# Kernel optimization log

Measured on AMD Instinct MI355X. Metric: run time of the kernel, lower is better.

## Reference

```python
import jax, jax.numpy as jnp
import numpy as np

B, C, H, W = 8, 512, 64, 64
K = 8  # shrink factor: qk channels = C//K, v channels = C//2


def conv1x1(x, w, b):
    # x: [B,C_in,H,W], w: [C_out,C_in], b: [C_out]  (1x1 conv == channel matmul)
    return jnp.einsum('bchw,oc->bohw', x, w) + b[None, :, None, None]


def maxpool2x2(x):
    b, c, h, w = x.shape
    return x.reshape(b, c, h // 2, 2, w // 2, 2).max(axis=(3, 5))


def setup_inputs() -> dict:
    key = jax.random.key(0)
    ks = jax.random.split(key, 9)
    Cqk, Cv = C // K, C // 2
    sc = lambda fan_in: 1.0 / np.sqrt(fan_in)
    return {
        'x': jax.random.normal(ks[0], (B, C, H, W), jnp.float32),
        'Wf': jax.random.normal(ks[1], (Cqk, C), jnp.float32) * sc(C),
        'bf': jnp.zeros((Cqk,), jnp.float32),
        'Wg': jax.random.normal(ks[2], (Cqk, C), jnp.float32) * sc(C),
        'bg': jnp.zeros((Cqk,), jnp.float32),
        'Wh': jax.random.normal(ks[3], (Cv, C), jnp.float32) * sc(C),
        'bh': jnp.zeros((Cv,), jnp.float32),
        'Wv': jax.random.normal(ks[4], (C, Cv), jnp.float32) * sc(Cv),
        'bv': jnp.zeros((C,), jnp.float32),
        'gamma': jnp.float32(0.5),
    }


def reference(x, Wf, bf, Wg, bg, Wh, bh, Wv, bv, gamma):
    b, c, h, w = x.shape
    f = conv1x1(x, Wf, bf).reshape(b, c // K, h * w)          # [B, C/K, HW]
    g = maxpool2x2(conv1x1(x, Wg, bg))                         # [B, C/K, H/2, W/2]
    v = maxpool2x2(conv1x1(x, Wh, bh))                         # [B, C/2, H/2, W/2]
    hwp = (h // 2) * (w // 2)
    g = g.reshape(b, c // K, hwp)
    v = v.reshape(b, c // 2, hwp)
    # s[b, n, m] = sum_c f[b,c,n] g[b,c,m]; softmax over m (no scaling, per SAGAN)
    s = jnp.einsum('bcn,bcm->bnm', f, g)                       # [B, HW, HW']
    beta = jax.nn.softmax(s, axis=-1)
    o = jnp.einsum('bcm,bnm->bcn', v, beta).reshape(b, c // 2, h, w)
    return gamma * conv1x1(o, Wv, bv) + x
```

## Files before the change

### kernel.cpp

```cpp
#include <hip/hip_runtime.h>
#include <cstddef>

typedef __attribute__((ext_vector_type(4))) float f32x4;
typedef __attribute__((ext_vector_type(16))) float f32x16;
typedef __attribute__((ext_vector_type(8))) short bf16x8;

#define MFMA16(A, B, C) __builtin_amdgcn_mfma_f32_16x16x32_bf16(A, B, C, 0, 0, 0)
#define MFMA32(A, B, C) __builtin_amdgcn_mfma_f32_32x32x16_bf16(A, B, C, 0, 0, 0)

__device__ __forceinline__ unsigned short f2bf(float f) {
  unsigned u = __float_as_uint(f);
  u += 0x7fffu + ((u >> 16) & 1u);
  return (unsigned short)(u >> 16);
}
__device__ __forceinline__ float bf2f(unsigned short s) {
  return __uint_as_float(((unsigned)s) << 16);
}

__device__ __forceinline__ void cvt_split8(float4 a, float4 b, bf16x8* H, bf16x8* L) {
  float v[8] = {a.x, a.y, a.z, a.w, b.x, b.y, b.z, b.w};
  unsigned hh[4], ll[4];
  #pragma unroll
  for (int p = 0; p < 4; ++p) {
    unsigned short h0 = f2bf(v[2 * p]), h1 = f2bf(v[2 * p + 1]);
    hh[p] = (unsigned)h0 | ((unsigned)h1 << 16);
    unsigned short l0 = f2bf(v[2 * p] - bf2f(h0));
    unsigned short l1 = f2bf(v[2 * p + 1] - bf2f(h1));
    ll[p] = (unsigned)l0 | ((unsigned)l1 << 16);
  }
  uint4 uh; uh.x = hh[0]; uh.y = hh[1]; uh.z = hh[2]; uh.w = hh[3];
  uint4 ul; ul.x = ll[0]; ul.y = ll[1]; ul.z = ll[2]; ul.w = ll[3];
  *H = *(bf16x8*)&uh;
  *L = *(bf16x8*)&ul;
}

__device__ __forceinline__ bf16x8 cvt_hi8(float4 a, float4 b) {
  float v[8] = {a.x, a.y, a.z, a.w, b.x, b.y, b.z, b.w};
  unsigned hh[4];
  #pragma unroll
  for (int p = 0; p < 4; ++p)
    hh[p] = (unsigned)f2bf(v[2 * p]) | ((unsigned)f2bf(v[2 * p + 1]) << 16);
  uint4 uh; uh.x = hh[0]; uh.y = hh[1]; uh.z = hh[2]; uh.w = hh[3];
  return *(bf16x8*)&uh;
}


__global__ void prep_k(const float* __restrict__ Wf, const float* __restrict__ Wg,
                       const float* __restrict__ Wh, const float* __restrict__ Wv,
                       unsigned short* __restrict__ wfh, unsigned short* __restrict__ wfl,
                       unsigned short* __restrict__ wgh, unsigned short* __restrict__ wgl,
                       unsigned short* __restrict__ whb, unsigned short* __restrict__ wvb) {
  int i = blockIdx.x * 256 + threadIdx.x;
  if (i < 65536) {
    int ii = i & 32767;
    int j = ii & 7, slot = (ii >> 3) & 63, q = slot & 15, qt2 = slot >> 4;
    int kt = (ii >> 9) & 15, oct = ii >> 13;
    const float* src = (i < 32768) ? Wf : Wg;
    unsigned short* dh = (i < 32768) ? wfh : wgh;
    unsigned short* dl = (i < 32768) ? wfl : wgl;
    float v = src[(oct * 16 + q) * 512 + kt * 32 + qt2 * 8 + j];
    unsigned short h = f2bf(v);
    dh[ii] = h; dl[ii] = f2bf(v - bf2f(h));
  } else if (i < 196608) {
    int ii = i - 65536;
    int j = ii & 7, slot = (ii >> 3) & 63, q = slot & 15, qt2 = slot >> 4;
    int kt = (ii >> 9) & 15, oct = ii >> 13;
    whb[ii] = f2bf(Wh[(oct * 16 + q) * 512 + kt * 32 + qt2 * 8 + j]);
  } else if (i < 327680) {
    int ii = i - 196608;
    int j = ii & 7, slot = (ii >> 3) & 63, q = slot & 15, qt2 = slot >> 4;
    int kt = (ii >> 9) & 7, oct = ii >> 12;
    wvb[ii] = f2bf(Wv[(oct * 16 + q) * 256 + kt * 32 + qt2 * 8 + j]);
  }
}


#define STAGE(BUF, CN) { _Pragma("unroll") \
  for (int c_ = 0; c_ < 8; ++c_) { \
    __builtin_amdgcn_global_load_lds( \
      (const __attribute__((address_space(1))) unsigned int*)(xg + (size_t)((CN) * 64 + c_ * 2) * 4096), \
      (__attribute__((address_space(3))) unsigned int*)(&xs[BUF][w * 16 + c_ * 2][0]), \
      16, 0, 0); } }

__global__ __launch_bounds__(256, 2)
void conv_all(const float* __restrict__ x,
              const unsigned short* __restrict__ wfh_, const unsigned short* __restrict__ wfl_,
              const unsigned short* __restrict__ wgh_, const unsigned short* __restrict__ wgl_,
              const unsigned short* __restrict__ whb_,
              const float* __restrict__ bf_, const float* __restrict__ bg_,
              const float* __restrict__ bh_,
              unsigned short* __restrict__ fhi, unsigned short* __restrict__ flo,
              unsigned short* __restrict__ ghi, unsigned short* __restrict__ glo,
              unsigned short* __restrict__ vp)
{
  __shared__ __align__(16) float xs[2][64][128];
  const int bid = blockIdx.x;
  const int b = bid & 7;
  const int idx = bid >> 3;
  const int role = idx & 1;
  const int hp = idx >> 1;
  const int n0 = hp * 128;
  const int tid = threadIdx.x, w = tid >> 6, lane = tid & 63, q = lane & 15, qt = lane >> 4;
  const float* xg = x + ((size_t)(b * 512 + w * 16 + (lane >> 5)) * 4096) + n0 + (lane & 31) * 4;

  if (role == 0) {
    f32x4 accf[2][4], accg[2][4];
    #pragma unroll
    for (int nt = 0; nt < 2; ++nt)
      #pragma unroll
      for (int ot = 0; ot < 4; ++ot) {
        accf[nt][ot] = (f32x4){0.f, 0.f, 0.f, 0.f};
        accg[nt][ot] = (f32x4){0.f, 0.f, 0.f, 0.f};
      }
    STAGE(0, 0)
    __syncthreads();
    for (int cc = 0; cc < 8; ++cc) {
      const int cur = cc & 1;
      if (cc < 7) STAGE(cur ^ 1, cc + 1)
      #pragma unroll
      for (int kh = 0; kh < 2; ++kh) {
        const int kt = cc * 2 + kh;
        bf16x8 Ah[2], Al[2];
        #pragma unroll
        for (int nt = 0; nt < 2; ++nt) {
          const int row = w * 32 + nt * 16 + q;
          float xv[8];
          #pragma unroll
          for (int j = 0; j < 8; ++j)
            xv[j] = xs[cur][kh * 32 + qt * 8 + j][row];
          float4 a0; a0.x = xv[0]; a0.y = xv[1]; a0.z = xv[2]; a0.w = xv[3];
          float4 a1; a1.x = xv[4]; a1.y = xv[5]; a1.z = xv[6]; a1.w = xv[7];
          cvt_split8(a0, a1, &Ah[nt], &Al[nt]);
        }
        {
          bf16x8 Bh[4], Bl[4];
          #pragma unroll
          for (int ot = 0; ot < 4; ++ot) {
            size_t wb = ((size_t)(ot * 16 + kt) << 9) + lane * 8;
            Bh[ot] = *(const bf16x8*)(wfh_ + wb);
            Bl[ot] = *(const bf16x8*)(wfl_ + wb);
          }
          #pragma unroll
          for (int nt = 0; nt < 2; ++nt)
            #pragma unroll
            for (int ot = 0; ot < 4; ++ot) {
              accf[nt][ot] = MFMA16(Ah[nt], Bh[ot], accf[nt][ot]);
              accf[nt][ot] = MFMA16(Ah[nt], Bl[ot], accf[nt][ot]);
              accf[nt][ot] = MFMA16(Al[nt], Bh[ot], accf[nt][ot]);
            }
        }
        {
          bf16x8 Bh[4], Bl[4];
          #pragma unroll
          for (int ot = 0; ot < 4; ++ot) {
            size_t wb = ((size_t)(ot * 16 + kt) << 9) + lane * 8;
            Bh[ot] = *(const bf16x8*)(wgh_ + wb);
            Bl[ot] = *(const bf16x8*)(wgl_ + wb);
          }
          #pragma unroll
          for (int nt = 0; nt < 2; ++nt)
            #pragma unroll
            for (int ot = 0; ot < 4; ++ot) {
              accg[nt][ot] = MFMA16(Ah[nt], Bh[ot], accg[nt][ot]);
              accg[nt][ot] = MFMA16(Ah[nt], Bl[ot], accg[nt][ot]);
              accg[nt][ot] = MFMA16(Al[nt], Bh[ot], accg[nt][ot]);
            }
        }
      }
      __syncthreads();
    }
    #pragma unroll
    for (int nt = 0; nt < 2; ++nt)
      #pragma unroll
      for (int ot = 0; ot < 4; ++ot)
        #pragma unroll
        for (int r = 0; r < 4; ++r) {
          float v = accf[nt][ot][r] + bf_[ot * 16 + q];
          unsigned short h = f2bf(v);
          size_t o = (((size_t)(b * 128 + hp * 4 + w) * 4 + ot) * 64 +
                      (q >> 3) * 32 + nt * 16 + qt * 4 + r) * 8 + (q & 7);
          fhi[o] = h;
          flo[o] = f2bf(v - bf2f(h));
        }
    float (*pl)[67] = (float(*)[67])&xs[0][0][0];
    #pragma unroll
    for (int nt = 0; nt < 2; ++nt)
      #pragma unroll
      for (int ot = 0; ot < 4; ++ot)
        #pragma unroll
        for (int r = 0; r < 4; ++r)
          pl[w * 32 + nt * 16 + qt * 4 + r][ot * 16 + q] = accg[nt][ot][r];
    __syncthreads();
    const int c = tid & 63;
    #pragma unroll
    for (int it = 0; it < 8; ++it) {
      int wp = (tid >> 6) + it * 4;
      float v = fmaxf(fmaxf(pl[2 * wp][c], pl[2 * wp + 1][c]),
                      fmaxf(pl[64 + 2 * wp][c], pl[65 + 2 * wp][c])) + bg_[c];
      unsigned short h = f2bf(v);
      size_t o = (((size_t)(b * 32 + hp) * 4 + (c >> 4)) * 64 +
                  ((c >> 3) & 1) * 32 + wp) * 8 + (c & 7);
      ghi[o] = h;
      glo[o] = f2bf(v - bf2f(h));
    }
  } else {
    f32x4 acc[2][16];
    #pragma unroll
    for (int nt = 0; nt < 2; ++nt)
      #pragma unroll
      for (int ot = 0; ot < 16; ++ot) acc[nt][ot] = (f32x4){0.f, 0.f, 0.f, 0.f};
    STAGE(0, 0)
    __syncthreads();
    for (int cc = 0; cc < 8; ++cc) {
      const int cur = cc & 1;
      if (cc < 7) STAGE(cur ^ 1, cc + 1)
      #pragma unroll
      for (int kh = 0; kh < 2; ++kh) {
        const int kt = cc * 2 + kh;
        bf16x8 A_[2];
        #pragma unroll
        for (int nt = 0; nt < 2; ++nt) {
          const int row = w * 32 + nt * 16 + q;
          float xv[8];
          #pragma unroll
          for (int j = 0; j < 8; ++j)
            xv[j] = xs[cur][kh * 32 + qt * 8 + j][row];
          float4 a0; a0.x = xv[0]; a0.y = xv[1]; a0.z = xv[2]; a0.w = xv[3];
          float4 a1; a1.x = xv[4]; a1.y = xv[5]; a1.z = xv[6]; a1.w = xv[7];
          A_[nt] = cvt_hi8(a0, a1);
        }
        #pragma unroll
        for (int oh = 0; oh < 2; ++oh) {
          bf16x8 B_[8];
          #pragma unroll
          for (int ot = 0; ot < 8; ++ot)
            B_[ot] = *(const bf16x8*)(whb_ + ((size_t)((oh * 8 + ot) * 16 + kt) << 9) + lane * 8);
          #pragma unroll
          for (int nt = 0; nt < 2; ++nt)
            #pragma unroll
            for (int ot = 0; ot < 8; ++ot)
              acc[nt][oh * 8 + ot] = MFMA16(A_[nt], B_[ot], acc[nt][oh * 8 + ot]);
        }
      }
      __syncthreads();
    }
    float (*pl)[67] = (float(*)[67])&xs[0][0][0];
    #pragma unroll
    for (int oh = 0; oh < 4; ++oh) {
      if (oh) __syncthreads();
      #pragma unroll
      for (int nt = 0; nt < 2; ++nt)
        #pragma unroll
        for (int ot4 = 0; ot4 < 4; ++ot4)
          #pragma unroll
          for (int r = 0; r < 4; ++r)
            pl[w * 32 + nt * 16 + qt * 4 + r][ot4 * 16 + q] = acc[nt][oh * 4 + ot4][r];
      __syncthreads();
      const int wp = tid & 31;
      #pragma unroll
      for (int it = 0; it < 8; ++it) {
        int cc2 = (tid >> 5) + it * 8;
        int cv = oh * 64 + cc2;
        float v = fmaxf(fmaxf(pl[2 * wp][cc2], pl[2 * wp + 1][cc2]),
                        fmaxf(pl[64 + 2 * wp][cc2], pl[65 + 2 * wp][cc2])) + bh_[cv];
        size_t o = (((size_t)(b * 16 + (cv >> 4)) * 32 + hp) * 64 +
                    (wp >> 3) * 16 + (cv & 15)) * 8 + (wp & 7);
        vp[o] = f2bf(v);
      }
    }
  }
}


#define PROW 264

__global__ __launch_bounds__(256, 2)
void attn_mfma(const unsigned short* __restrict__ f_, const unsigned short* __restrict__ fl_,
               const unsigned short* __restrict__ g_, const unsigned short* __restrict__ gl_,
               const unsigned short* __restrict__ vp, unsigned short* __restrict__ oT)
{
  __shared__ __align__(16) unsigned short PB[64 * PROW];
  __shared__ float redm[4][2][32], reds[4][2][32];
  const int b = blockIdx.x & 7, bx = blockIdx.x >> 3;
  const int tid = threadIdx.x, w = tid >> 6, lane = tid & 63;
  const int q32 = lane & 31, hl = lane >> 5;
  const int q16 = lane & 15, qt = lane >> 4;

  bf16x8 Fh[2][4], Fl[2][4];
  #pragma unroll
  for (int qt2 = 0; qt2 < 2; ++qt2) {
    size_t fb = ((size_t)(b * 128 + bx * 2 + qt2) << 11) + lane * 8;
    #pragma unroll
    for (int s = 0; s < 4; ++s) {
      Fh[qt2][s] = *(const bf16x8*)(f_ + fb + (s << 9));
      Fl[qt2][s] = *(const bf16x8*)(fl_ + fb + (s << 9));
    }
  }

  float M0 = -3.0e38f, M1 = -3.0e38f;
  float Mp[4], Sp[4];
  #pragma unroll
  for (int qs = 0; qs < 4; ++qs) { Mp[qs] = -3.0e38f; Sp[qs] = 0.f; }
  f32x4 oacc[4][4];
  #pragma unroll
  for (int c4 = 0; c4 < 4; ++c4)
    #pragma unroll
    for (int qs = 0; qs < 4; ++qs) oacc[c4][qs] = (f32x4){0.f, 0.f, 0.f, 0.f};
  const size_t vroot = ((size_t)(b * 16 + w * 4) * 32) * 512 + lane * 8;

#define VLD(C4, KS) (*(const bf16x8*)(vp + vroot + ((size_t)((C4) * 32 + mc * 8 + (KS)) << 9)))
#define LOADVA(KS) { va0 = VLD(0, KS); va1 = VLD(1, KS); va2 = VLD(2, KS); va3 = VLD(3, KS); }
#define LOADVB(KS) { vb0 = VLD(0, KS); vb1 = VLD(1, KS); vb2 = VLD(2, KS); vb3 = VLD(3, KS); }
#define PVMFMA(KS, V0, V1, V2, V3) { \
  bf16x8 pb0 = *(const bf16x8*)&PB[q16 * PROW + (KS) * 32 + qt * 8]; \
  bf16x8 pb1 = *(const bf16x8*)&PB[(16 + q16) * PROW + (KS) * 32 + qt * 8]; \
  bf16x8 pb2 = *(const bf16x8*)&PB[(32 + q16) * PROW + (KS) * 32 + qt * 8]; \
  bf16x8 pb3 = *(const bf16x8*)&PB[(48 + q16) * PROW + (KS) * 32 + qt * 8]; \
  oacc[0][0] = MFMA16(V0, pb0, oacc[0][0]); oacc[1][0] = MFMA16(V1, pb0, oacc[1][0]); \
  oacc[2][0] = MFMA16(V2, pb0, oacc[2][0]); oacc[3][0] = MFMA16(V3, pb0, oacc[3][0]); \
  oacc[0][1] = MFMA16(V0, pb1, oacc[0][1]); oacc[1][1] = MFMA16(V1, pb1, oacc[1][1]); \
  oacc[2][1] = MFMA16(V2, pb1, oacc[2][1]); oacc[3][1] = MFMA16(V3, pb1, oacc[3][1]); \
  oacc[0][2] = MFMA16(V0, pb2, oacc[0][2]); oacc[1][2] = MFMA16(V1, pb2, oacc[1][2]); \
  oacc[2][2] = MFMA16(V2, pb2, oacc[2][2]); oacc[3][2] = MFMA16(V3, pb2, oacc[3][2]); \
  oacc[0][3] = MFMA16(V0, pb3, oacc[0][3]); oacc[1][3] = MFMA16(V1, pb3, oacc[1][3]); \
  oacc[2][3] = MFMA16(V2, pb3, oacc[2][3]); oacc[3][3] = MFMA16(V3, pb3, oacc[3][3]); }

  #pragma unroll 1
  for (int mc = 0; mc < 4; ++mc) {
    f32x16 sa0t0 = {}, sa0t1 = {}, sa1t0 = {}, sa1t1 = {};
    __builtin_amdgcn_s_setprio(1);
    #pragma unroll
    for (int t = 0; t < 2; ++t) {
      size_t gb = ((size_t)(b * 32 + mc * 8 + w * 2 + t) << 11) + lane * 8;
      bf16x8 Gh[4], Gl[4];
      #pragma unroll
      for (int s = 0; s < 4; ++s) {
        Gh[s] = *(const bf16x8*)(g_ + gb + (s << 9));
        Gl[s] = *(const bf16x8*)(gl_ + gb + (s << 9));
      }
      f32x16* s0 = t ? &sa0t1 : &sa0t0;
      f32x16* s1 = t ? &sa1t1 : &sa1t0;
      #pragma unroll
      for (int s = 0; s < 4; ++s) {
        *s0 = MFMA32(Gh[s], Fh[0][s], *s0);
        *s0 = MFMA32(Gh[s], Fl[0][s], *s0);
        *s0 = MFMA32(Gl[s], Fh[0][s], *s0);
        *s1 = MFMA32(Gh[s], Fh[1][s], *s1);
        *s1 = MFMA32(Gh[s], Fl[1][s], *s1);
        *s1 = MFMA32(Gl[s], Fh[1][s], *s1);
      }
    }
    __builtin_amdgcn_s_setprio(0);

    bf16x8 va0, va1, va2, va3, vb0, vb1, vb2, vb3;
    LOADVA(0)

    float mx0 = -3.0e38f, mx1 = -3.0e38f;
    #pragma unroll
    for (int r = 0; r < 16; ++r) {
      mx0 = fmaxf(mx0, fmaxf(sa0t0[r], sa0t1[r]));
      mx1 = fmaxf(mx1, fmaxf(sa1t0[r], sa1t1[r]));
    }
    mx0 = fmaxf(mx0, __shfl_xor(mx0, 32));
    mx1 = fmaxf(mx1, __shfl_xor(mx1, 32));
    if (lane < 32) { redm[w][0][lane] = mx0; redm[w][1][lane] = mx1; }
    __syncthreads();
    float gmx0 = fmaxf(fmaxf(redm[0][0][q32], redm[1][0][q32]), fmaxf(redm[2][0][q32], redm[3][0][q32]));
    float gmx1 = fmaxf(fmaxf(redm[0][1][q32], redm[1][1][q32]), fmaxf(redm[2][1][q32], redm[3][1][q32]));
    float Mn0 = fmaxf(M0, gmx0), Mn1 = fmaxf(M1, gmx1);
    M0 = Mn0; M1 = Mn1;

    float rfp[4];
    #pragma unroll
    for (int qs = 0; qs < 4; ++qs) {
      int hq = qs >> 1, cq = (qs & 1) * 16 + q16;
      float gm = fmaxf(fmaxf(redm[0][hq][cq], redm[1][hq][cq]),
                       fmaxf(redm[2][hq][cq], redm[3][hq][cq]));
      float Mn = fmaxf(Mp[qs], gm);
      rfp[qs] = __expf(Mp[qs] - Mn);
      Mp[qs] = Mn;
    }

    float cs0 = 0.f, cs1 = 0.f;
    #pragma unroll
    for (int r = 0; r < 16; ++r) {
      float p;
      p = __expf(sa0t0[r] - Mn0); sa0t0[r] = p; cs0 += p;
      p = __expf(sa0t1[r] - Mn0); sa0t1[r] = p; cs0 += p;
      p = __expf(sa1t0[r] - Mn1); sa1t0[r] = p; cs1 += p;
      p = __expf(sa1t1[r] - Mn1); sa1t1[r] = p; cs1 += p;
    }
    cs0 += __shfl_xor(cs0, 32);
    cs1 += __shfl_xor(cs1, 32);
    if (lane < 32) { reds[w][0][lane] = cs0; reds[w][1][lane] = cs1; }

    #pragma unroll
    for (int j = 0; j < 4; ++j) {
      uint2 pk;
      pk.x = (unsigned)f2bf(sa0t0[4*j+0]) | ((unsigned)f2bf(sa0t0[4*j+1]) << 16);
      pk.y = (unsigned)f2bf(sa0t0[4*j+2]) | ((unsigned)f2bf(sa0t0[4*j+3]) << 16);
      *(uint2*)&PB[q32 * PROW + w * 64 + j * 8 + hl * 4] = pk;
      pk.x = (unsigned)f2bf(sa0t1[4*j+0]) | ((unsigned)f2bf(sa0t1[4*j+1]) << 16);
      pk.y = (unsigned)f2bf(sa0t1[4*j+2]) | ((unsigned)f2bf(sa0t1[4*j+3]) << 16);
      *(uint2*)&PB[q32 * PROW + w * 64 + 32 + j * 8 + hl * 4] = pk;
      pk.x = (unsigned)f2bf(sa1t0[4*j+0]) | ((unsigned)f2bf(sa1t0[4*j+1]) << 16);
      pk.y = (unsigned)f2bf(sa1t0[4*j+2]) | ((unsigned)f2bf(sa1t0[4*j+3]) << 16);
      *(uint2*)&PB[(32 + q32) * PROW + w * 64 + j * 8 + hl * 4] = pk;
      pk.x = (unsigned)f2bf(sa1t1[4*j+0]) | ((unsigned)f2bf(sa1t1[4*j+1]) << 16);
      pk.y = (unsigned)f2bf(sa1t1[4*j+2]) | ((unsigned)f2bf(sa1t1[4*j+3]) << 16);
      *(uint2*)&PB[(32 + q32) * PROW + w * 64 + 32 + j * 8 + hl * 4] = pk;
    }
    __syncthreads();

    #pragma unroll
    for (int qs = 0; qs < 4; ++qs) {
      int hq = qs >> 1, cq = (qs & 1) * 16 + q16;
      float ct = reds[0][hq][cq] + reds[1][hq][cq] + reds[2][hq][cq] + reds[3][hq][cq];
      Sp[qs] = (mc == 0) ? ct : Sp[qs] * rfp[qs] + ct;
    }

    if (mc > 0) {
      #pragma unroll
      for (int c4 = 0; c4 < 4; ++c4)
        #pragma unroll
        for (int qs = 0; qs < 4; ++qs) oacc[c4][qs] *= rfp[qs];
    }
    LOADVB(1)
    __builtin_amdgcn_s_setprio(1);
    #pragma unroll
    for (int kp = 0; kp < 4; ++kp) {
      PVMFMA(2 * kp, va0, va1, va2, va3)
      if (2 * kp + 2 < 8) LOADVA(2 * kp + 2)
      PVMFMA(2 * kp + 1, vb0, vb1, vb2, vb3)
      if (2 * kp + 3 < 8) LOADVB(2 * kp + 3)
    }
    __builtin_amdgcn_s_setprio(0);
  }

  __syncthreads();
  float rinv[4];
  #pragma unroll
  for (int qs = 0; qs < 4; ++qs) rinv[qs] = 1.0f / Sp[qs];
  #pragma unroll
  for (int c4 = 0; c4 < 4; ++c4)
    #pragma unroll
    for (int qs = 0; qs < 4; ++qs) {
      uint2 pk;
      pk.x = (unsigned)f2bf(oacc[c4][qs][0] * rinv[qs]) | ((unsigned)f2bf(oacc[c4][qs][1] * rinv[qs]) << 16);
      pk.y = (unsigned)f2bf(oacc[c4][qs][2] * rinv[qs]) | ((unsigned)f2bf(oacc[c4][qs][3] * rinv[qs]) << 16);
      *(uint2*)&PB[(qs * 16 + q16) * PROW + w * 64 + c4 * 16 + qt * 4] = pk;
    }
  __syncthreads();
  const size_t obase = (size_t)(b * 256 + bx * 4) * 4096;
  #pragma unroll
  for (int it = 0; it < 8; ++it) {
    int u = it * 256 + tid;
    int so = u * 8;
    int ntl = so >> 12;
    int rem = so & 4095;
    int ks = rem >> 9;
    int slot = (rem >> 3) & 63;
    int qq = slot & 15, cg = slot >> 4;
    uint4 val = *(const uint4*)&PB[(ntl * 16 + qq) * PROW + ks * 32 + cg * 8];
    *(uint4*)(oT + obase + so) = val;
  }
}


__global__ __launch_bounds__(256)
void conv_final(const unsigned short* __restrict__ A, const unsigned short* __restrict__ W,
                const float* __restrict__ bias, float* __restrict__ out,
                const float* __restrict__ resid, const float* __restrict__ gamma_p)
{
  const int bid = blockIdx.x;
  const int b = bid & 7;
  const int idx = bid >> 3;
  const int n0 = (idx & 31) * 128;
  const int oc0 = (idx >> 5) * 128;
  const int tid = threadIdx.x, w = tid >> 6, lane = tid & 63, q = lane & 15, qt = lane >> 4;

  f32x4 acc[2][8];
  #pragma unroll
  for (int nt = 0; nt < 2; ++nt)
    #pragma unroll
    for (int ot = 0; ot < 8; ++ot) acc[nt][ot] = (f32x4){0.f, 0.f, 0.f, 0.f};

  #pragma unroll
  for (int ks = 0; ks < 8; ++ks) {
    bf16x8 A_[2], B_[8];
    #pragma unroll
    for (int nt = 0; nt < 2; ++nt)
      A_[nt] = *(const bf16x8*)(A + (((size_t)(b * 256 + (n0 >> 4) + w * 2 + nt) * 8 + ks) << 9) + lane * 8);
    #pragma unroll
    for (int ot = 0; ot < 8; ++ot)
      B_[ot] = *(const bf16x8*)(W + (((size_t)((oc0 >> 4) + ot) * 8 + ks) << 9) + lane * 8);
    #pragma unroll
    for (int nt = 0; nt < 2; ++nt)
      #pragma unroll
      for (int ot = 0; ot < 8; ++ot)
        acc[nt][ot] = MFMA16(A_[nt], B_[ot], acc[nt][ot]);
  }

  const float gm = gamma_p[0];
  #pragma unroll
  for (int ot = 0; ot < 8; ++ot) {
    int oc = oc0 + ot * 16 + q;
    float bs = bias[oc];
    #pragma unroll
    for (int nt = 0; nt < 2; ++nt) {
      int n = n0 + w * 32 + nt * 16 + qt * 4;
      size_t o = ((size_t)(b * 512) + oc) * 4096 + n;
      float4 rs = *(const float4*)&resid[o];
      float4 ov;
      ov.x = gm * (acc[nt][ot][0] + bs) + rs.x;
      ov.y = gm * (acc[nt][ot][1] + bs) + rs.y;
      ov.z = gm * (acc[nt][ot][2] + bs) + rs.z;
      ov.w = gm * (acc[nt][ot][3] + bs) + rs.w;
      *(float4*)&out[o] = ov;
    }
  }
}


extern "C" void kernel_launch(void* const* d_in, const int* in_sizes, int n_in,
                              void* d_out, int out_size, void* d_ws, size_t ws_size,
                              hipStream_t stream) {
  const float* x     = (const float*)d_in[0];
  const float* Wf    = (const float*)d_in[1];
  const float* bf    = (const float*)d_in[2];
  const float* Wg    = (const float*)d_in[3];
  const float* bg    = (const float*)d_in[4];
  const float* Wh    = (const float*)d_in[5];
  const float* bh    = (const float*)d_in[6];
  const float* Wv    = (const float*)d_in[7];
  const float* bv    = (const float*)d_in[8];
  const float* gamma = (const float*)d_in[9];
  float* out = (float*)d_out;
  char* w = (char*)d_ws;

  unsigned short* fhi = (unsigned short*)(w);
  unsigned short* flo = (unsigned short*)(w + 4194304);
  unsigned short* ghi = (unsigned short*)(w + 8388608);
  unsigned short* glo = (unsigned short*)(w + 9437184);
  unsigned short* vp  = (unsigned short*)(w + 10485760);
  unsigned short* oT  = (unsigned short*)(w + 14680064);
  unsigned short* wfh = (unsigned short*)(w + 31457280);
  unsigned short* wfl = (unsigned short*)(w + 31522816);
  unsigned short* wgh = (unsigned short*)(w + 31588352);
  unsigned short* wgl = (unsigned short*)(w + 31653888);
  unsigned short* whb = (unsigned short*)(w + 31719424);
  unsigned short* wvb = (unsigned short*)(w + 31981568);

  prep_k<<<1280, 256, 0, stream>>>(Wf, Wg, Wh, Wv, wfh, wfl, wgh, wgl, whb, wvb);

  conv_all<<<512, 256, 0, stream>>>(x, wfh, wfl, wgh, wgl, whb,
                                    bf, bg, bh, fhi, flo, ghi, glo, vp);

  attn_mfma<<<512, 256, 0, stream>>>(fhi, flo, ghi, glo, vp, oT);

  conv_final<<<1024, 256, 0, stream>>>(oT, wvb, bv, out, x, gamma);
}
```

Baseline: 111.3 us.

## Halve attention query tile to 32 rows and double grid for occupancy

The attention kernel now processes 32 query rows per block instead of 64, so it launches twice as many blocks, uses half the LDS and fewer accumulator registers, and raises the launch bound to 3 blocks per CU. The goal is better latency hiding and wave occupancy. In exchange, each block reloads the full G and V streams for half the queries, so global and L2 traffic for K/V doubles and each MFMA has less reuse.

Result: slower. 116.7 us (+4.8%).

```diff
diff --git a/kernel.cpp b/kernel.cpp
--- a/kernel.cpp
+++ b/kernel.cpp
@@ -274,38 +274,37 @@
 
 #define PROW 264
 
-__global__ __launch_bounds__(256, 2)
+__global__ __launch_bounds__(256, 3)
 void attn_mfma(const unsigned short* __restrict__ f_, const unsigned short* __restrict__ fl_,
                const unsigned short* __restrict__ g_, const unsigned short* __restrict__ gl_,
                const unsigned short* __restrict__ vp, unsigned short* __restrict__ oT)
 {
-  __shared__ __align__(16) unsigned short PB[64 * PROW];
-  __shared__ float redm[4][2][32], reds[4][2][32];
+  __shared__ __align__(16) unsigned short PB[32 * PROW];
+  __shared__ float redm[4][32], reds[4][32];
   const int b = blockIdx.x & 7, bx = blockIdx.x >> 3;
   const int tid = threadIdx.x, w = tid >> 6, lane = tid & 63;
   const int q32 = lane & 31, hl = lane >> 5;
   const int q16 = lane & 15, qt = lane >> 4;
 
-  bf16x8 Fh[2][4], Fl[2][4];
-  #pragma unroll
-  for (int qt2 = 0; qt2 < 2; ++qt2) {
-    size_t fb = ((size_t)(b * 128 + bx * 2 + qt2) << 11) + lane * 8;
+  bf16x8 Fh[4], Fl[4];
+  {
+    size_t fb = ((size_t)(b * 128 + bx) << 11) + lane * 8;
     #pragma unroll
     for (int s = 0; s < 4; ++s) {
-      Fh[qt2][s] = *(const bf16x8*)(f_ + fb + (s << 9));
-      Fl[qt2][s] = *(const bf16x8*)(fl_ + fb + (s << 9));
-    }
-  }
-
-  float M0 = -3.0e38f, M1 = -3.0e38f;
-  float Mp[4], Sp[4];
-  #pragma unroll
-  for (int qs = 0; qs < 4; ++qs) { Mp[qs] = -3.0e38f; Sp[qs] = 0.f; }
-  f32x4 oacc[4][4];
+      Fh[s] = *(const bf16x8*)(f_ + fb + (s << 9));
+      Fl[s] = *(const bf16x8*)(fl_ + fb + (s << 9));
+    }
+  }
+
+  float M0 = -3.0e38f;
+  float Mp[2], Sp[2];
+  #pragma unroll
+  for (int qs = 0; qs < 2; ++qs) { Mp[qs] = -3.0e38f; Sp[qs] = 0.f; }
+  f32x4 oacc[4][2];
   #pragma unroll
   for (int c4 = 0; c4 < 4; ++c4)
     #pragma unroll
-    for (int qs = 0; qs < 4; ++qs) oacc[c4][qs] = (f32x4){0.f, 0.f, 0.f, 0.f};
+    for (int qs = 0; qs < 2; ++qs) oacc[c4][qs] = (f32x4){0.f, 0.f, 0.f, 0.f};
   const size_t vroot = ((size_t)(b * 16 + w * 4) * 32) * 512 + lane * 8;
 
 #define VLD(C4, KS) (*(const bf16x8*)(vp + vroot + ((size_t)((C4) * 32 + mc * 8 + (KS)) << 9)))
@@ -314,20 +313,14 @@
 #define PVMFMA(KS, V0, V1, V2, V3) { \
   bf16x8 pb0 = *(const bf16x8*)&PB[q16 * PROW + (KS) * 32 + qt * 8]; \
   bf16x8 pb1 = *(const bf16x8*)&PB[(16 + q16) * PROW + (KS) * 32 + qt * 8]; \
-  bf16x8 pb2 = *(const bf16x8*)&PB[(32 + q16) * PROW + (KS) * 32 + qt * 8]; \
-  bf16x8 pb3 = *(const bf16x8*)&PB[(48 + q16) * PROW + (KS) * 32 + qt * 8]; \
   oacc[0][0] = MFMA16(V0, pb0, oacc[0][0]); oacc[1][0] = MFMA16(V1, pb0, oacc[1][0]); \
   oacc[2][0] = MFMA16(V2, pb0, oacc[2][0]); oacc[3][0] = MFMA16(V3, pb0, oacc[3][0]); \
   oacc[0][1] = MFMA16(V0, pb1, oacc[0][1]); oacc[1][1] = MFMA16(V1, pb1, oacc[1][1]); \
-  oacc[2][1] = MFMA16(V2, pb1, oacc[2][1]); oacc[3][1] = MFMA16(V3, pb1, oacc[3][1]); \
-  oacc[0][2] = MFMA16(V0, pb2, oacc[0][2]); oacc[1][2] = MFMA16(V1, pb2, oacc[1][2]); \
-  oacc[2][2] = MFMA16(V2, pb2, oacc[2][2]); oacc[3][2] = MFMA16(V3, pb2, oacc[3][2]); \
-  oacc[0][3] = MFMA16(V0, pb3, oacc[0][3]); oacc[1][3] = MFMA16(V1, pb3, oacc[1][3]); \
-  oacc[2][3] = MFMA16(V2, pb3, oacc[2][3]); oacc[3][3] = MFMA16(V3, pb3, oacc[3][3]); }
+  oacc[2][1] = MFMA16(V2, pb1, oacc[2][1]); oacc[3][1] = MFMA16(V3, pb1, oacc[3][1]); }
 
   #pragma unroll 1
   for (int mc = 0; mc < 4; ++mc) {
-    f32x16 sa0t0 = {}, sa0t1 = {}, sa1t0 = {}, sa1t1 = {};
+    f32x16 sat0 = {}, sat1 = {};
     __builtin_amdgcn_s_setprio(1);
     #pragma unroll
     for (int t = 0; t < 2; ++t) {
@@ -338,16 +331,12 @@
         Gh[s] = *(const bf16x8*)(g_ + gb + (s << 9));
         Gl[s] = *(const bf16x8*)(gl_ + gb + (s << 9));
       }
-      f32x16* s0 = t ? &sa0t1 : &sa0t0;
-      f32x16* s1 = t ? &sa1t1 : &sa1t0;
+      f32x16* s0 = t ? &sat1 : &sat0;
       #pragma unroll
       for (int s = 0; s < 4; ++s) {
-        *s0 = MFMA32(Gh[s], Fh[0][s], *s0);
-        *s0 = MFMA32(Gh[s], Fl[0][s], *s0);
-        *s0 = MFMA32(Gl[s], Fh[0][s], *s0);
-        *s1 = MFMA32(Gh[s], Fh[1][s], *s1);
-        *s1 = MFMA32(Gh[s], Fl[1][s], *s1);
-        *s1 = MFMA32(Gl[s], Fh[1][s], *s1);
+        *s0 = MFMA32(Gh[s], Fh[s], *s0);
+        *s0 = MFMA32(Gh[s], Fl[s], *s0);
+        *s0 = MFMA32(Gl[s], Fh[s], *s0);
       }
     }
     __builtin_amdgcn_s_setprio(0);
@@ -355,67 +344,54 @@
     bf16x8 va0, va1, va2, va3, vb0, vb1, vb2, vb3;
     LOADVA(0)
 
-    float mx0 = -3.0e38f, mx1 = -3.0e38f;
-    #pragma unroll
-    for (int r = 0; r < 16; ++r) {
-      mx0 = fmaxf(mx0, fmaxf(sa0t0[r], sa0t1[r]));
-      mx1 = fmaxf(mx1, fmaxf(sa1t0[r], sa1t1[r]));
-    }
+    float mx0 = -3.0e38f;
+    #pragma unroll
+    for (int r = 0; r < 16; ++r)
+      mx0 = fmaxf(mx0, fmaxf(sat0[r], sat1[r]));
     mx0 = fmaxf(mx0, __shfl_xor(mx0, 32));
-    mx1 = fmaxf(mx1, __shfl_xor(mx1, 32));
-    if (lane < 32) { redm[w][0][lane] = mx0; redm[w][1][lane] = mx1; }
+    if (lane < 32) redm[w][lane] = mx0;
     __syncthreads();
-    float gmx0 = fmaxf(fmaxf(redm[0][0][q32], redm[1][0][q32]), fmaxf(redm[2][0][q32], redm[3][0][q32]));
-    float gmx1 = fmaxf(fmaxf(redm[0][1][q32], redm[1][1][q32]), fmaxf(redm[2][1][q32], redm[3][1][q32]));
-    float Mn0 = fmaxf(M0, gmx0), Mn1 = fmaxf(M1, gmx1);
-    M0 = Mn0; M1 = Mn1;
-
-    float rfp[4];
-    #pragma unroll
-    for (int qs = 0; qs < 4; ++qs) {
-      int hq = qs >> 1, cq = (qs & 1) * 16 + q16;
-      float gm = fmaxf(fmaxf(redm[0][hq][cq], redm[1][hq][cq]),
-                       fmaxf(redm[2][hq][cq], redm[3][hq][cq]));
+    float gmx0 = fmaxf(fmaxf(redm[0][q32], redm[1][q32]), fmaxf(redm[2][q32], redm[3][q32]));
+    float Mn0 = fmaxf(M0, gmx0);
+    M0 = Mn0;
+
+    float rfp[2];
+    #pragma unroll
+    for (int qs = 0; qs < 2; ++qs) {
+      int cq = qs * 16 + q16;
+      float gm = fmaxf(fmaxf(redm[0][cq], redm[1][cq]),
+                       fmaxf(redm[2][cq], redm[3][cq]));
       float Mn = fmaxf(Mp[qs], gm);
       rfp[qs] = __expf(Mp[qs] - Mn);
       Mp[qs] = Mn;
     }
 
-    float cs0 = 0.f, cs1 = 0.f;
+    float cs0 = 0.f;
     #pragma unroll
     for (int r = 0; r < 16; ++r) {
       float p;
-      p = __expf(sa0t0[r] - Mn0); sa0t0[r] = p; cs0 += p;
-      p = __expf(sa0t1[r] - Mn0); sa0t1[r] = p; cs0 += p;
-      p = __expf(sa1t0[r] - Mn1); sa1t0[r] = p; cs1 += p;
-      p = __expf(sa1t1[r] - Mn1); sa1t1[r] = p; cs1 += p;
+      p = __expf(sat0[r] - Mn0); sat0[r] = p; cs0 += p;
+      p = __expf(sat1[r] - Mn0); sat1[r] = p; cs0 += p;
     }
     cs0 += __shfl_xor(cs0, 32);
-    cs1 += __shfl_xor(cs1, 32);
-    if (lane < 32) { reds[w][0][lane] = cs0; reds[w][1][lane] = cs1; }
+    if (lane < 32) reds[w][lane] = cs0;
 
     #pragma unroll
     for (int j = 0; j < 4; ++j) {
       uint2 pk;
-      pk.x = (unsigned)f2bf(sa0t0[4*j+0]) | ((unsigned)f2bf(sa0t0[4*j+1]) << 16);
-      pk.y = (unsigned)f2bf(sa0t0[4*j+2]) | ((unsigned)f2bf(sa0t0[4*j+3]) << 16);
+      pk.x = (unsigned)f2bf(sat0[4*j+0]) | ((unsigned)f2bf(sat0[4*j+1]) << 16);
+      pk.y = (unsigned)f2bf(sat0[4*j+2]) | ((unsigned)f2bf(sat0[4*j+3]) << 16);
       *(uint2*)&PB[q32 * PROW + w * 64 + j * 8 + hl * 4] = pk;
-      pk.x = (unsigned)f2bf(sa0t1[4*j+0]) | ((unsigned)f2bf(sa0t1[4*j+1]) << 16);
-      pk.y = (unsigned)f2bf(sa0t1[4*j+2]) | ((unsigned)f2bf(sa0t1[4*j+3]) << 16);
+      pk.x = (unsigned)f2bf(sat1[4*j+0]) | ((unsigned)f2bf(sat1[4*j+1]) << 16);
+      pk.y = (unsigned)f2bf(sat1[4*j+2]) | ((unsigned)f2bf(sat1[4*j+3]) << 16);
       *(uint2*)&PB[q32 * PROW + w * 64 + 32 + j * 8 + hl * 4] = pk;
-      pk.x = (unsigned)f2bf(sa1t0[4*j+0]) | ((unsigned)f2bf(sa1t0[4*j+1]) << 16);
-      pk.y = (unsigned)f2bf(sa1t0[4*j+2]) | ((unsigned)f2bf(sa1t0[4*j+3]) << 16);
-      *(uint2*)&PB[(32 + q32) * PROW + w * 64 + j * 8 + hl * 4] = pk;
-      pk.x = (unsigned)f2bf(sa1t1[4*j+0]) | ((unsigned)f2bf(sa1t1[4*j+1]) << 16);
-      pk.y = (unsigned)f2bf(sa1t1[4*j+2]) | ((unsigned)f2bf(sa1t1[4*j+3]) << 16);
-      *(uint2*)&PB[(32 + q32) * PROW + w * 64 + 32 + j * 8 + hl * 4] = pk;
     }
     __syncthreads();
 
     #pragma unroll
-    for (int qs = 0; qs < 4; ++qs) {
-      int hq = qs >> 1, cq = (qs & 1) * 16 + q16;
-      float ct = reds[0][hq][cq] + reds[1][hq][cq] + reds[2][hq][cq] + reds[3][hq][cq];
+    for (int qs = 0; qs < 2; ++qs) {
+      int cq = qs * 16 + q16;
+      float ct = reds[0][cq] + reds[1][cq] + reds[2][cq] + reds[3][cq];
       Sp[qs] = (mc == 0) ? ct : Sp[qs] * rfp[qs] + ct;
     }
 
@@ -423,7 +399,7 @@
       #pragma unroll
       for (int c4 = 0; c4 < 4; ++c4)
         #pragma unroll
-        for (int qs = 0; qs < 4; ++qs) oacc[c4][qs] *= rfp[qs];
+        for (int qs = 0; qs < 2; ++qs) oacc[c4][qs] *= rfp[qs];
     }
     LOADVB(1)
     __builtin_amdgcn_s_setprio(1);
@@ -438,22 +414,22 @@
   }
 
   __syncthreads();
-  float rinv[4];
-  #pragma unroll
-  for (int qs = 0; qs < 4; ++qs) rinv[qs] = 1.0f / Sp[qs];
+  float rinv[2];
+  #pragma unroll
+  for (int qs = 0; qs < 2; ++qs) rinv[qs] = 1.0f / Sp[qs];
   #pragma unroll
   for (int c4 = 0; c4 < 4; ++c4)
     #pragma unroll
-    for (int qs = 0; qs < 4; ++qs) {
+    for (int qs = 0; qs < 2; ++qs) {
       uint2 pk;
       pk.x = (unsigned)f2bf(oacc[c4][qs][0] * rinv[qs]) | ((unsigned)f2bf(oacc[c4][qs][1] * rinv[qs]) << 16);
       pk.y = (unsigned)f2bf(oacc[c4][qs][2] * rinv[qs]) | ((unsigned)f2bf(oacc[c4][qs][3] * rinv[qs]) << 16);
       *(uint2*)&PB[(qs * 16 + q16) * PROW + w * 64 + c4 * 16 + qt * 4] = pk;
     }
   __syncthreads();
-  const size_t obase = (size_t)(b * 256 + bx * 4) * 4096;
-  #pragma unroll
-  for (int it = 0; it < 8; ++it) {
+  const size_t obase = (size_t)(b * 256 + bx * 2) * 4096;
+  #pragma unroll
+  for (int it = 0; it < 4; ++it) {
     int u = it * 256 + tid;
     int so = u * 8;
     int ntl = so >> 12;
@@ -556,7 +532,7 @@
   conv_all<<<512, 256, 0, stream>>>(x, wfh, wfl, wgh, wgl, whb,
                                     bf, bg, bh, fhi, flo, ghi, glo, vp);
 
-  attn_mfma<<<512, 256, 0, stream>>>(fhi, flo, ghi, glo, vp, oT);
+  attn_mfma<<<1024, 256, 0, stream>>>(fhi, flo, ghi, glo, vp, oT);
 
   conv_final<<<1024, 256, 0, stream>>>(oT, wvb, bv, out, x, gamma);
 }
```

## Stage conv weight tiles into LDS via async global_load_lds alongside x

Applied to the files above, without the earlier changes.

The conv kernel used to read bf16 weight fragments directly from global memory inside the MFMA loop. It now copies each K-slice of weights into double-buffered LDS with global_load_lds, in step with the x tiles. The K chunk is halved to 32 channels per stage, giving 16 iterations instead of 8, so the same 64KB of LDS holds both x and weight buffers. This is meant to hide weight-load latency behind compute, at the cost of more barriers per K pass and a different LDS footprint.

Result: no change. 110.4 us (-0.8%).

```diff
diff --git a/kernel.cpp b/kernel.cpp
--- a/kernel.cpp
+++ b/kernel.cpp
@@ -7,6 +7,8 @@
 
 #define MFMA16(A, B, C) __builtin_amdgcn_mfma_f32_16x16x32_bf16(A, B, C, 0, 0, 0)
 #define MFMA32(A, B, C) __builtin_amdgcn_mfma_f32_32x32x16_bf16(A, B, C, 0, 0, 0)
+#define AS1 __attribute__((address_space(1)))
+#define AS3 __attribute__((address_space(3)))
 
 __device__ __forceinline__ unsigned short f2bf(float f) {
   unsigned u = __float_as_uint(f);
@@ -75,12 +77,25 @@
 }
 
 
-#define STAGE(BUF, CN) { _Pragma("unroll") \
-  for (int c_ = 0; c_ < 8; ++c_) { \
+#define STAGEX(XP, CN) { _Pragma("unroll") \
+  for (int c_ = 0; c_ < 4; ++c_) \
     __builtin_amdgcn_global_load_lds( \
-      (const __attribute__((address_space(1))) unsigned int*)(xg + (size_t)((CN) * 64 + c_ * 2) * 4096), \
-      (__attribute__((address_space(3))) unsigned int*)(&xs[BUF][w * 16 + c_ * 2][0]), \
-      16, 0, 0); } }
+      (const AS1 unsigned int*)(xg + (size_t)((CN) * 32 + c_ * 2) * 4096), \
+      (AS3 unsigned int*)((XP) + (w * 8 + c_ * 2) * 128), 16, 0, 0); }
+
+#define STAGEW0(WP, CN) { \
+  const unsigned short* Wt_ = (w == 0) ? wfh_ : (w == 1) ? wfl_ : (w == 2) ? wgh_ : wgl_; \
+  _Pragma("unroll") \
+  for (int ot_ = 0; ot_ < 4; ++ot_) \
+    __builtin_amdgcn_global_load_lds( \
+      (const AS1 unsigned int*)(Wt_ + (((size_t)(ot_ * 16 + (CN))) << 9) + lane * 8), \
+      (AS3 unsigned int*)((WP) + (w * 4 + ot_) * 512), 16, 0, 0); }
+
+#define STAGEW1(WP, CN) { _Pragma("unroll") \
+  for (int i_ = 0; i_ < 4; ++i_) \
+    __builtin_amdgcn_global_load_lds( \
+      (const AS1 unsigned int*)(whb_ + (((size_t)((w * 4 + i_) * 16 + (CN))) << 9) + lane * 8), \
+      (AS3 unsigned int*)((WP) + (w * 4 + i_) * 512), 16, 0, 0); }
 
 __global__ __launch_bounds__(256, 2)
 void conv_all(const float* __restrict__ x,
@@ -93,7 +108,11 @@
               unsigned short* __restrict__ ghi, unsigned short* __restrict__ glo,
               unsigned short* __restrict__ vp)
 {
-  __shared__ __align__(16) float xs[2][64][128];
+  __shared__ __align__(16) char smem[65536];
+  float* xs0 = (float*)smem;
+  float* xs1 = (float*)(smem + 16384);
+  unsigned short* ws0 = (unsigned short*)(smem + 32768);
+  unsigned short* ws1 = (unsigned short*)(smem + 49152);
   const int bid = blockIdx.x;
   const int b = bid & 7;
   const int idx = bid >> 3;
@@ -101,7 +120,7 @@
   const int hp = idx >> 1;
   const int n0 = hp * 128;
   const int tid = threadIdx.x, w = tid >> 6, lane = tid & 63, q = lane & 15, qt = lane >> 4;
-  const float* xg = x + ((size_t)(b * 512 + w * 16 + (lane >> 5)) * 4096) + n0 + (lane & 31) * 4;
+  const float* xg = x + ((size_t)(b * 512 + w * 8 + (lane >> 5)) * 4096) + n0 + (lane & 31) * 4;
 
   if (role == 0) {
     f32x4 accf[2][4], accg[2][4];
@@ -112,60 +131,57 @@
         accf[nt][ot] = (f32x4){0.f, 0.f, 0.f, 0.f};
         accg[nt][ot] = (f32x4){0.f, 0.f, 0.f, 0.f};
       }
-    STAGE(0, 0)
+    STAGEX(xs0, 0) STAGEW0(ws0, 0)
     __syncthreads();
-    for (int cc = 0; cc < 8; ++cc) {
-      const int cur = cc & 1;
-      if (cc < 7) STAGE(cur ^ 1, cc + 1)
-      #pragma unroll
-      for (int kh = 0; kh < 2; ++kh) {
-        const int kt = cc * 2 + kh;
-        bf16x8 Ah[2], Al[2];
-        #pragma unroll
-        for (int nt = 0; nt < 2; ++nt) {
-          const int row = w * 32 + nt * 16 + q;
-          float xv[8];
-          #pragma unroll
-          for (int j = 0; j < 8; ++j)
-            xv[j] = xs[cur][kh * 32 + qt * 8 + j][row];
-          float4 a0; a0.x = xv[0]; a0.y = xv[1]; a0.z = xv[2]; a0.w = xv[3];
-          float4 a1; a1.x = xv[4]; a1.y = xv[5]; a1.z = xv[6]; a1.w = xv[7];
-          cvt_split8(a0, a1, &Ah[nt], &Al[nt]);
+    for (int cc = 0; cc < 16; ++cc) {
+      const float* xsp = (cc & 1) ? xs1 : xs0;
+      const unsigned short* wp = (cc & 1) ? ws1 : ws0;
+      float* xsn = (cc & 1) ? xs0 : xs1;
+      unsigned short* wn = (cc & 1) ? ws0 : ws1;
+      if (cc < 15) { STAGEX(xsn, cc + 1) STAGEW0(wn, cc + 1) }
+      bf16x8 Ah[2], Al[2];
+      #pragma unroll
+      for (int nt = 0; nt < 2; ++nt) {
+        const int row = w * 32 + nt * 16 + q;
+        float xv[8];
+        #pragma unroll
+        for (int j = 0; j < 8; ++j)
+          xv[j] = xsp[(qt * 8 + j) * 128 + row];
+        float4 a0; a0.x = xv[0]; a0.y = xv[1]; a0.z = xv[2]; a0.w = xv[3];
+        float4 a1; a1.x = xv[4]; a1.y = xv[5]; a1.z = xv[6]; a1.w = xv[7];
+        cvt_split8(a0, a1, &Ah[nt], &Al[nt]);
+      }
+      {
+        bf16x8 Bh[4], Bl[4];
+        #pragma unroll
+        for (int ot = 0; ot < 4; ++ot) {
+          Bh[ot] = *(const bf16x8*)&wp[(0 + ot) * 512 + lane * 8];
+          Bl[ot] = *(const bf16x8*)&wp[(4 + ot) * 512 + lane * 8];
         }
-        {
-          bf16x8 Bh[4], Bl[4];
+        #pragma unroll
+        for (int nt = 0; nt < 2; ++nt)
           #pragma unroll
           for (int ot = 0; ot < 4; ++ot) {
-            size_t wb = ((size_t)(ot * 16 + kt) << 9) + lane * 8;
-            Bh[ot] = *(const bf16x8*)(wfh_ + wb);
-            Bl[ot] = *(const bf16x8*)(wfl_ + wb);
+            accf[nt][ot] = MFMA16(Ah[nt], Bh[ot], accf[nt][ot]);
+            accf[nt][ot] = MFMA16(Ah[nt], Bl[ot], accf[nt][ot]);
+            accf[nt][ot] = MFMA16(Al[nt], Bh[ot], accf[nt][ot]);
           }
-          #pragma unroll
-          for (int nt = 0; nt < 2; ++nt)
-            #pragma unroll
-            for (int ot = 0; ot < 4; ++ot) {
-              accf[nt][ot] = MFMA16(Ah[nt], Bh[ot], accf[nt][ot]);
-              accf[nt][ot] = MFMA16(Ah[nt], Bl[ot], accf[nt][ot]);
-              accf[nt][ot] = MFMA16(Al[nt], Bh[ot], accf[nt][ot]);
-            }
+      }
+      {
+        bf16x8 Bh[4], Bl[4];
+        #pragma unroll
+        for (int ot = 0; ot < 4; ++ot) {
+          Bh[ot] = *(const bf16x8*)&wp[(8 + ot) * 512 + lane * 8];
+          Bl[ot] = *(const bf16x8*)&wp[(12 + ot) * 512 + lane * 8];
         }
-        {
-          bf16x8 Bh[4], Bl[4];
+        #pragma unroll
+        for (int nt = 0; nt < 2; ++nt)
           #pragma unroll
           for (int ot = 0; ot < 4; ++ot) {
-            size_t wb = ((size_t)(ot * 16 + kt) << 9) + lane * 8;
-            Bh[ot] = *(const bf16x8*)(wgh_ + wb);
-            Bl[ot] = *(const bf16x8*)(wgl_ + wb);
+            accg[nt][ot] = MFMA16(Ah[nt], Bh[ot], accg[nt][ot]);
+            accg[nt][ot] = MFMA16(Ah[nt], Bl[ot], accg[nt][ot]);
+            accg[nt][ot] = MFMA16(Al[nt], Bh[ot], accg[nt][ot]);
           }
-          #pragma unroll
-          for (int nt = 0; nt < 2; ++nt)
-            #pragma unroll
-            for (int ot = 0; ot < 4; ++ot) {
-              accg[nt][ot] = MFMA16(Ah[nt], Bh[ot], accg[nt][ot]);
-              accg[nt][ot] = MFMA16(Ah[nt], Bl[ot], accg[nt][ot]);
-              accg[nt][ot] = MFMA16(Al[nt], Bh[ot], accg[nt][ot]);
-            }
-        }
       }
       __syncthreads();
     }
@@ -182,7 +198,7 @@
           fhi[o] = h;
           flo[o] = f2bf(v - bf2f(h));
         }
-    float (*pl)[67] = (float(*)[67])&xs[0][0][0];
+    float (*pl)[67] = (float(*)[67])smem;
     #pragma unroll
     for (int nt = 0; nt < 2; ++nt)
       #pragma unroll
@@ -194,12 +210,12 @@
     const int c = tid & 63;
     #pragma unroll
     for (int it = 0; it < 8; ++it) {
-      int wp = (tid >> 6) + it * 4;
-      float v = fmaxf(fmaxf(pl[2 * wp][c], pl[2 * wp + 1][c]),
-                      fmaxf(pl[64 + 2 * wp][c], pl[65 + 2 * wp][c])) + bg_[c];
+      int wp2 = (tid >> 6) + it * 4;
+      float v = fmaxf(fmaxf(pl[2 * wp2][c], pl[2 * wp2 + 1][c]),
+                      fmaxf(pl[64 + 2 * wp2][c], pl[65 + 2 * wp2][c])) + bg_[c];
       unsigned short h = f2bf(v);
       size_t o = (((size_t)(b * 32 + hp) * 4 + (c >> 4)) * 64 +
-                  ((c >> 3) & 1) * 32 + wp) * 8 + (c & 7);
+                  ((c >> 3) & 1) * 32 + wp2) * 8 + (c & 7);
       ghi[o] = h;
       glo[o] = f2bf(v - bf2f(h));
     }
@@ -209,42 +225,41 @@
     for (int nt = 0; nt < 2; ++nt)
       #pragma unroll
       for (int ot = 0; ot < 16; ++ot) acc[nt][ot] = (f32x4){0.f, 0.f, 0.f, 0.f};
-    STAGE(0, 0)
+    STAGEX(xs0, 0) STAGEW1(ws0, 0)
     __syncthreads();
-    for (int cc = 0; cc < 8; ++cc) {
-      const int cur = cc & 1;
-      if (cc < 7) STAGE(cur ^ 1, cc + 1)
-      #pragma unroll
-      for (int kh = 0; kh < 2; ++kh) {
-        const int kt = cc * 2 + kh;
-        bf16x8 A_[2];
-        #pragma unroll
-        for (int nt = 0; nt < 2; ++nt) {
-          const int row = w * 32 + nt * 16 + q;
-          float xv[8];
-          #pragma unroll
-          for (int j = 0; j < 8; ++j)
-            xv[j] = xs[cur][kh * 32 + qt * 8 + j][row];
-          float4 a0; a0.x = xv[0]; a0.y = xv[1]; a0.z = xv[2]; a0.w = xv[3];
-          float4 a1; a1.x = xv[4]; a1.y = xv[5]; a1.z = xv[6]; a1.w = xv[7];
-          A_[nt] = cvt_hi8(a0, a1);
-        }
-        #pragma unroll
-        for (int oh = 0; oh < 2; ++oh) {
-          bf16x8 B_[8];
+    for (int cc = 0; cc < 16; ++cc) {
+      const float* xsp = (cc & 1) ? xs1 : xs0;
+      const unsigned short* wp = (cc & 1) ? ws1 : ws0;
+      float* xsn = (cc & 1) ? xs0 : xs1;
+      unsigned short* wn = (cc & 1) ? ws0 : ws1;
+      if (cc < 15) { STAGEX(xsn, cc + 1) STAGEW1(wn, cc + 1) }
+      bf16x8 A_[2];
+      #pragma unroll
+      for (int nt = 0; nt < 2; ++nt) {
+        const int row = w * 32 + nt * 16 + q;
+        float xv[8];
+        #pragma unroll
+        for (int j = 0; j < 8; ++j)
+          xv[j] = xsp[(qt * 8 + j) * 128 + row];
+        float4 a0; a0.x = xv[0]; a0.y = xv[1]; a0.z = xv[2]; a0.w = xv[3];
+        float4 a1; a1.x = xv[4]; a1.y = xv[5]; a1.z = xv[6]; a1.w = xv[7];
+        A_[nt] = cvt_hi8(a0, a1);
+      }
+      #pragma unroll
+      for (int oh = 0; oh < 2; ++oh) {
+        bf16x8 B_[8];
+        #pragma unroll
+        for (int ot = 0; ot < 8; ++ot)
+          B_[ot] = *(const bf16x8*)&wp[(oh * 8 + ot) * 512 + lane * 8];
+        #pragma unroll
+        for (int nt = 0; nt < 2; ++nt)
           #pragma unroll
           for (int ot = 0; ot < 8; ++ot)
-            B_[ot] = *(const bf16x8*)(whb_ + ((size_t)((oh * 8 + ot) * 16 + kt) << 9) + lane * 8);
-          #pragma unroll
-          for (int nt = 0; nt < 2; ++nt)
-            #pragma unroll
-            for (int ot = 0; ot < 8; ++ot)
-              acc[nt][oh * 8 + ot] = MFMA16(A_[nt], B_[ot], acc[nt][oh * 8 + ot]);
-        }
+            acc[nt][oh * 8 + ot] = MFMA16(A_[nt], B_[ot], acc[nt][oh * 8 + ot]);
       }
       __syncthreads();
     }
-    float (*pl)[67] = (float(*)[67])&xs[0][0][0];
+    float (*pl)[67] = (float(*)[67])smem;
     #pragma unroll
     for (int oh = 0; oh < 4; ++oh) {
       if (oh) __syncthreads();
@@ -256,15 +271,15 @@
           for (int r = 0; r < 4; ++r)
             pl[w * 32 + nt * 16 + qt * 4 + r][ot4 * 16 + q] = acc[nt][oh * 4 + ot4][r];
       __syncthreads();
-      const int wp = tid & 31;
+      const int wp2 = tid & 31;
       #pragma unroll
       for (int it = 0; it < 8; ++it) {
         int cc2 = (tid >> 5) + it * 8;
         int cv = oh * 64 + cc2;
-        float v = fmaxf(fmaxf(pl[2 * wp][cc2], pl[2 * wp + 1][cc2]),
-                        fmaxf(pl[64 + 2 * wp][cc2], pl[65 + 2 * wp][cc2])) + bh_[cv];
+        float v = fmaxf(fmaxf(pl[2 * wp2][cc2], pl[2 * wp2 + 1][cc2]),
+                        fmaxf(pl[64 + 2 * wp2][cc2], pl[65 + 2 * wp2][cc2])) + bh_[cv];
         size_t o = (((size_t)(b * 16 + (cv >> 4)) * 32 + hp) * 64 +
-                    (wp >> 3) * 16 + (cv & 15)) * 8 + (wp & 7);
+                    (wp2 >> 3) * 16 + (cv & 15)) * 8 + (wp2 & 7);
         vp[o] = f2bf(v);
       }
     }
```
